# Optimization experiments

Hardware: AMD Instinct MI355X
Metric: run time of the kernel (lower is better)

## Reference

```python
import jax, jax.numpy as jnp
import numpy as np


def _maxpool2(t):
    # 2x2 max pool, stride 2. t: [B, C, H, W]
    B, C, H, W = t.shape
    return t.reshape(B, C, H // 2, 2, W // 2, 2).max(axis=(3, 5))


def setup_inputs() -> dict:
    key = jax.random.key(0)
    ks = jax.random.split(key, 5)
    B, C, H, W = 4, 64, 128, 128
    x = jax.random.normal(ks[0], (B, C, H, W), dtype=jnp.float32)
    w_theta = jax.random.normal(ks[1], (C // 8, C), dtype=jnp.float32) * (1.0 / np.sqrt(C))
    w_phi = jax.random.normal(ks[2], (C // 8, C), dtype=jnp.float32) * (1.0 / np.sqrt(C))
    w_g = jax.random.normal(ks[3], (C // 2, C), dtype=jnp.float32) * (1.0 / np.sqrt(C))
    w_o = jax.random.normal(ks[4], (C, C // 2), dtype=jnp.float32) * (1.0 / np.sqrt(C // 2))
    gamma = jnp.ones((1,), dtype=jnp.float32)
    return {"x": x, "w_theta": w_theta, "w_phi": w_phi, "w_g": w_g, "w_o": w_o, "gamma": gamma}


def reference(x, w_theta, w_phi, w_g, w_o, gamma):
    B, C, H, W = x.shape
    N = H * W
    # 1x1 convs (bias-free) are channel matmuls
    theta = jnp.einsum('oc,bchw->bohw', w_theta, x)            # [B, C/8, H, W]
    phi = _maxpool2(jnp.einsum('oc,bchw->bohw', w_phi, x))     # [B, C/8, H/2, W/2]
    g = _maxpool2(jnp.einsum('oc,bchw->bohw', w_g, x))         # [B, C/2, H/2, W/2]
    theta = theta.reshape(B, C // 8, N)                        # [B, C/8, N]
    phi = phi.reshape(B, C // 8, N // 4)                       # [B, C/8, N/4]
    g = g.reshape(B, C // 2, N // 4)                           # [B, C/2, N/4]
    # attention: no 1/sqrt(d) scaling in SAGAN
    scores = jnp.einsum('bcn,bcm->bnm', theta, phi)            # [B, N, N/4]
    beta = jax.nn.softmax(scores, axis=-1)
    attn = jnp.einsum('bcm,bnm->bcn', g, beta)                 # [B, C/2, N]
    o = jnp.einsum('oc,bcn->bon', w_o, attn).reshape(B, C, H, W)
    return gamma[0] * o + x
```

## Files before the change

kernel.cpp:

```cpp
#include <hip/hip_runtime.h>
#include <hip/hip_bf16.h>


typedef __attribute__((ext_vector_type(4))) float f32x4;
typedef __attribute__((ext_vector_type(8))) short s16x8;
typedef __attribute__((ext_vector_type(4))) short s16x4;

__device__ __forceinline__ unsigned short f32_bf16(float f) {
    unsigned int u = __float_as_uint(f);
    return (unsigned short)((u + 0x7fffu + ((u >> 16) & 1u)) >> 16);
}
__device__ __forceinline__ unsigned int pk_bf16(float a, float b) {
    return (unsigned int)f32_bf16(a) | ((unsigned int)f32_bf16(b) << 16);
}
__device__ __forceinline__ unsigned int pk_rh(float a, float b) {
    unsigned int au = __float_as_uint(a) + 0x8000u;
    unsigned int bu = __float_as_uint(b) + 0x8000u;
    return __builtin_amdgcn_perm(bu, au, 0x07060302u);
}
__device__ __forceinline__ unsigned int pk_tr(float a, float b) {
    return __builtin_amdgcn_perm(__float_as_uint(b), __float_as_uint(a), 0x07060302u);
}
__device__ __forceinline__ void async16(const void* g, void* l) {
    __builtin_amdgcn_global_load_lds(
        (const __attribute__((address_space(1))) unsigned int*)g,
        (__attribute__((address_space(3))) unsigned int*)l, 16, 0, 0);
}

__global__ __launch_bounds__(256) void proj_kernel(
    const float* __restrict__ x,
    const float* __restrict__ w_theta, const float* __restrict__ w_phi,
    const float* __restrict__ w_g,
    __hip_bfloat16* __restrict__ thG,
    __hip_bfloat16* __restrict__ phG,
    __hip_bfloat16* __restrict__ gG)
{
    __shared__ __align__(16) unsigned short x_s[128 * 72];
    int tid = threadIdx.x;
    int bx = blockIdx.x;
    int b = bx >> 7, mh = (bx >> 1) & 63, ph = bx & 1;

    {
        int cp = tid >> 3, s = tid & 7;
        const float* xb = x + ((size_t)b << 20) + (size_t)(2 * mh) * 128 + 64 * ph;
        const float* p0r = xb + ((size_t)(2 * cp) << 14);
        const float* p1r = p0r + (1 << 14);
#pragma unroll
        for (int py = 0; py < 2; py++)
#pragma unroll
            for (int t = 0; t < 2; t++) {
                int pxl = 4 * s + 32 * t;
                float4 a = *(const float4*)(p0r + py * 128 + pxl);
                float4 c = *(const float4*)(p1r + py * 128 + pxl);
                int pix = py * 64 + pxl;
                *(unsigned int*)&x_s[(pix + 0) * 72 + 2 * cp] = pk_rh(a.x, c.x);
                *(unsigned int*)&x_s[(pix + 1) * 72 + 2 * cp] = pk_rh(a.y, c.y);
                *(unsigned int*)&x_s[(pix + 2) * 72 + 2 * cp] = pk_rh(a.z, c.z);
                *(unsigned int*)&x_s[(pix + 3) * 72 + 2 * cp] = pk_rh(a.w, c.w);
            }
    }

    int lane = tid & 63, w = tid >> 6;
    int q = lane >> 4, nl = lane & 15;

    s16x8 A[3][2];
#pragma unroll
    for (int CT = 0; CT < 3; CT++) {
        const float* wsrc;
        float scale = 1.0f;
        if (CT == 0) {
            if (nl < 8) { wsrc = w_theta + nl * 64; scale = 1.44269504f; }
            else        { wsrc = w_phi + (nl - 8) * 64; }
        } else if (CT == 1) wsrc = w_g + nl * 64;
        else                wsrc = w_g + (16 + nl) * 64;
#pragma unroll
        for (int ks = 0; ks < 2; ks++) {
            const float4* p4 = (const float4*)(wsrc + 32 * ks + 8 * q);
            float4 a0 = p4[0], a1 = p4[1];
            s16x8 f;
            f[0] = (short)f32_bf16(a0.x * scale); f[1] = (short)f32_bf16(a0.y * scale);
            f[2] = (short)f32_bf16(a0.z * scale); f[3] = (short)f32_bf16(a0.w * scale);
            f[4] = (short)f32_bf16(a1.x * scale); f[5] = (short)f32_bf16(a1.y * scale);
            f[6] = (short)f32_bf16(a1.z * scale); f[7] = (short)f32_bf16(a1.w * scale);
            A[CT][ks] = f;
        }
    }
    __syncthreads();

    f32x4 acc[3][2];
#pragma unroll
    for (int ti = 0; ti < 2; ti++) {
        int tile = w + 4 * ti;
        const unsigned short* rb = x_s + (16 * tile + nl) * 72;
        s16x8 B0 = *(const s16x8*)(rb + 8 * q);
        s16x8 B1 = *(const s16x8*)(rb + 32 + 8 * q);
#pragma unroll
        for (int CT = 0; CT < 3; CT++) {
            f32x4 d = (f32x4){0.f, 0.f, 0.f, 0.f};
            d = __builtin_amdgcn_mfma_f32_16x16x32_bf16(A[CT][0], B0, d, 0, 0, 0);
            d = __builtin_amdgcn_mfma_f32_16x16x32_bf16(A[CT][1], B1, d, 0, 0, 0);
            acc[CT][ti] = d;
        }
    }

    if (q < 2) {
        unsigned short* thb = (unsigned short*)thG + ((size_t)b << 14) * 8;
#pragma unroll
        for (int ti = 0; ti < 2; ti++) {
            int n = (2 * mh + ti) * 128 + 64 * ph + 16 * w + nl;
            uint2 tv;
            tv.x = pk_bf16(acc[0][ti][0], acc[0][ti][1]);
            tv.y = pk_bf16(acc[0][ti][2], acc[0][ti][3]);
            *(uint2*)(thb + (size_t)n * 8 + 4 * q) = tv;
        }
    }

    float pool[3][4];
#pragma unroll
    for (int CT = 0; CT < 3; CT++)
#pragma unroll
        for (int r = 0; r < 4; r++) {
            float a = fmaxf(acc[CT][0][r], acc[CT][1][r]);
            pool[CT][r] = fmaxf(a, __shfl_xor(a, 1));
        }

    int mm = 8 * w + (nl >> 1);
    int mbase = mh * 64 + ph * 32;
    if ((nl & 1) == 0) {
        if (q >= 2) {
            uint2 pv;
            pv.x = pk_bf16(pool[0][0], pool[0][1]);
            pv.y = pk_bf16(pool[0][2], pool[0][3]);
            *(uint2*)((unsigned short*)phG + ((size_t)(b * 4096 + mbase + mm)) * 8 + (q - 2) * 4) = pv;
        }
        int p = 8 * ((mm >> 2) & 3) + 4 * ((mm >> 4) & 1) + (mm & 3);
        int mstore = mbase + p;
#pragma unroll
        for (int CT = 1; CT < 3; CT++)
#pragma unroll
            for (int r = 0; r < 4; r++) {
                int cg = 16 * (CT - 1) + 4 * q + r;
                ((unsigned short*)gG)[((size_t)(b * 32 + cg) << 12) + mstore] =
                    f32_bf16(pool[CT][r]);
            }
    }
}

__global__ __launch_bounds__(256) void attn_kernel(
    const __hip_bfloat16* __restrict__ thG, const __hip_bfloat16* __restrict__ phG,
    const __hip_bfloat16* __restrict__ gG,
    const float* __restrict__ w_o, const float* __restrict__ gamma,
    const float* __restrict__ x, float* __restrict__ out)
{
    __shared__ __align__(16) unsigned char smem[2 * 16384 + 2 * 4096];
    unsigned char* O_s = smem;

    int tid = threadIdx.x, lane = tid & 63, w = tid >> 6;
    int q = lane >> 4, nl = lane & 15;
    int bx = blockIdx.x;
    int b  = bx >> 7;
    int n0 = (bx & 127) << 7;
    int nw = n0 + w * 32;

    const unsigned short* thb = (const unsigned short*)thG + ((size_t)b << 14) * 8;
    const unsigned short* phb = (const unsigned short*)phG + ((size_t)b << 12) * 8;
    const unsigned short* ggb = (const unsigned short*)gG + ((size_t)b << 17);

    s16x8 BT0 = (s16x8){0, 0, 0, 0, 0, 0, 0, 0};
    s16x8 BT1 = (s16x8){0, 0, 0, 0, 0, 0, 0, 0};
    if (q == 0) {
        BT0 = *(const s16x8*)(thb + (size_t)(nw + nl) * 8);
        BT1 = *(const s16x8*)(thb + (size_t)(nw + 16 + nl) * 8);
    } else if (q == 1) {
        BT0[0] = (short)0xC167;
        BT1[0] = (short)0xC167;
    }
    s16x8 Fc = (s16x8){0, 0, 0, 0, 0, 0, 0, 0};
    if (q == 1) Fc[0] = (short)0x3F80;
    const s16x4 ONE4 = (s16x4){(short)0x3F80, (short)0x3F80, (short)0x3F80, (short)0x3F80};

    f32x4 acc00 = (f32x4){0.f, 0.f, 0.f, 0.f};
    f32x4 acc10 = (f32x4){0.f, 0.f, 0.f, 0.f};
    f32x4 acc01 = (f32x4){0.f, 0.f, 0.f, 0.f};
    f32x4 acc11 = (f32x4){0.f, 0.f, 0.f, 0.f};
    f32x4 accL0 = (f32x4){0.f, 0.f, 0.f, 0.f};
    f32x4 accL1 = (f32x4){0.f, 0.f, 0.f, 0.f};

    int r0 = 8 * w + (lane >> 5);
    const unsigned short* gsrc0 = ggb + ((size_t)(r0 + 0) << 12) + 8 * ((lane & 31) ^ (r0 + 0));
    const unsigned short* gsrc1 = ggb + ((size_t)(r0 + 2) << 12) + 8 * ((lane & 31) ^ (r0 + 2));
    const unsigned short* gsrc2 = ggb + ((size_t)(r0 + 4) << 12) + 8 * ((lane & 31) ^ (r0 + 4));
    const unsigned short* gsrc3 = ggb + ((size_t)(r0 + 6) << 12) + 8 * ((lane & 31) ^ (r0 + 6));
    const unsigned short* psrc  = phb + (size_t)(w * 64 + lane) * 8;
    unsigned char* ldsg0 = smem + w * 4096;
    unsigned char* ldsg1 = ldsg0 + 1024;
    unsigned char* ldsg2 = ldsg0 + 2048;
    unsigned char* ldsg3 = ldsg0 + 3072;
    unsigned char* ldsp  = smem + 32768 + w * 1024;

    async16(gsrc0, ldsg0);
    async16(gsrc1, ldsg1);
    async16(gsrc2, ldsg2);
    async16(gsrc3, ldsg3);
    async16(psrc, ldsp);
    __syncthreads();

    for (int st = 0; st < 16; st++) {
        const unsigned char* gcur = smem + (st & 1) * 16384;
        const unsigned char* pcur = smem + 32768 + (st & 1) * 4096;
        if (st < 15) {
            int mo = (st + 1) << 8;
            int nb = (st + 1) & 1;
            async16(gsrc0 + mo, ldsg0 + nb * 16384);
            async16(gsrc1 + mo, ldsg1 + nb * 16384);
            async16(gsrc2 + mo, ldsg2 + nb * 16384);
            async16(gsrc3 + mo, ldsg3 + nb * 16384);
            async16(psrc + (size_t)mo * 8, ldsp + nb * 4096);
        }
#pragma unroll
        for (int cc = 0; cc < 8; cc++) {
            int mloc = cc << 5;
            s16x8 F0 = Fc, F1 = Fc;
            if (q == 0) {
                F0 = *(const s16x8*)(pcur + (mloc + nl) * 16);
                F1 = *(const s16x8*)(pcur + (mloc + 16 + nl) * 16);
            }
            int t = (cc << 2) + q;
            s16x8 G0 = *(const s16x8*)(gcur + nl * 512 + ((t ^ nl) << 4));
            s16x8 G1 = *(const s16x8*)(gcur + (nl + 16) * 512 + ((t ^ (nl + 16)) << 4));

            f32x4 z = (f32x4){0.f, 0.f, 0.f, 0.f};
            f32x4 s00 = __builtin_amdgcn_mfma_f32_16x16x32_bf16(F0, BT0, z, 0, 0, 0);
            f32x4 s01 = __builtin_amdgcn_mfma_f32_16x16x32_bf16(F1, BT0, z, 0, 0, 0);
            f32x4 s10 = __builtin_amdgcn_mfma_f32_16x16x32_bf16(F0, BT1, z, 0, 0, 0);
            f32x4 s11 = __builtin_amdgcn_mfma_f32_16x16x32_bf16(F1, BT1, z, 0, 0, 0);

            float a0 = __builtin_amdgcn_exp2f(s00[0]);
            float a1 = __builtin_amdgcn_exp2f(s00[1]);
            float a2 = __builtin_amdgcn_exp2f(s00[2]);
            float a3 = __builtin_amdgcn_exp2f(s00[3]);
            float b0 = __builtin_amdgcn_exp2f(s01[0]);
            float b1 = __builtin_amdgcn_exp2f(s01[1]);
            float b2 = __builtin_amdgcn_exp2f(s01[2]);
            float b3 = __builtin_amdgcn_exp2f(s01[3]);
            float c0 = __builtin_amdgcn_exp2f(s10[0]);
            float c1 = __builtin_amdgcn_exp2f(s10[1]);
            float c2 = __builtin_amdgcn_exp2f(s10[2]);
            float c3 = __builtin_amdgcn_exp2f(s10[3]);
            float d0 = __builtin_amdgcn_exp2f(s11[0]);
            float d1 = __builtin_amdgcn_exp2f(s11[1]);
            float d2 = __builtin_amdgcn_exp2f(s11[2]);
            float d3 = __builtin_amdgcn_exp2f(s11[3]);

            uint2 u00 = make_uint2(pk_tr(a0, a1), pk_tr(a2, a3));
            uint2 u01 = make_uint2(pk_tr(b0, b1), pk_tr(b2, b3));
            uint2 u10 = make_uint2(pk_tr(c0, c1), pk_tr(c2, c3));
            uint2 u11 = make_uint2(pk_tr(d0, d1), pk_tr(d2, d3));
            s16x4 P00 = *(s16x4*)&u00;
            s16x4 P01 = *(s16x4*)&u01;
            s16x4 P10 = *(s16x4*)&u10;
            s16x4 P11 = *(s16x4*)&u11;

            accL0 = __builtin_amdgcn_mfma_f32_16x16x16bf16_1k(ONE4, P00, accL0, 0, 0, 0);
            accL0 = __builtin_amdgcn_mfma_f32_16x16x16bf16_1k(ONE4, P01, accL0, 0, 0, 0);
            accL1 = __builtin_amdgcn_mfma_f32_16x16x16bf16_1k(ONE4, P10, accL1, 0, 0, 0);
            accL1 = __builtin_amdgcn_mfma_f32_16x16x16bf16_1k(ONE4, P11, accL1, 0, 0, 0);

            s16x4 G0a = __builtin_shufflevector(G0, G0, 0, 1, 2, 3);
            s16x4 G0b = __builtin_shufflevector(G0, G0, 4, 5, 6, 7);
            s16x4 G1a = __builtin_shufflevector(G1, G1, 0, 1, 2, 3);
            s16x4 G1b = __builtin_shufflevector(G1, G1, 4, 5, 6, 7);
            acc00 = __builtin_amdgcn_mfma_f32_16x16x16bf16_1k(G0a, P00, acc00, 0, 0, 0);
            acc00 = __builtin_amdgcn_mfma_f32_16x16x16bf16_1k(G0b, P01, acc00, 0, 0, 0);
            acc10 = __builtin_amdgcn_mfma_f32_16x16x16bf16_1k(G1a, P00, acc10, 0, 0, 0);
            acc10 = __builtin_amdgcn_mfma_f32_16x16x16bf16_1k(G1b, P01, acc10, 0, 0, 0);
            acc01 = __builtin_amdgcn_mfma_f32_16x16x16bf16_1k(G0a, P10, acc01, 0, 0, 0);
            acc01 = __builtin_amdgcn_mfma_f32_16x16x16bf16_1k(G0b, P11, acc01, 0, 0, 0);
            acc11 = __builtin_amdgcn_mfma_f32_16x16x16bf16_1k(G1a, P10, acc11, 0, 0, 0);
            acc11 = __builtin_amdgcn_mfma_f32_16x16x16bf16_1k(G1b, P11, acc11, 0, 0, 0);
        }
        __syncthreads();
    }

    float li0 = 1.0f / accL0[0];
    float li1 = 1.0f / accL1[0];
    acc00 *= li0; acc10 *= li0;
    acc01 *= li1; acc11 *= li1;

    s16x8 WO[4];
#pragma unroll
    for (int g4 = 0; g4 < 4; g4++) {
        const float4* wr = (const float4*)(w_o + (size_t)(g4 * 16 + nl) * 32 + q * 8);
        float4 a0 = wr[0], a1 = wr[1];
        WO[g4][0] = (short)f32_bf16(a0.x); WO[g4][1] = (short)f32_bf16(a0.y);
        WO[g4][2] = (short)f32_bf16(a0.z); WO[g4][3] = (short)f32_bf16(a0.w);
        WO[g4][4] = (short)f32_bf16(a1.x); WO[g4][5] = (short)f32_bf16(a1.y);
        WO[g4][6] = (short)f32_bf16(a1.z); WO[g4][7] = (short)f32_bf16(a1.w);
    }
    float gam = gamma[0];

    int nloc0 = w * 32 + nl;
    int nloc1 = nloc0 + 16;
    {
        uint2 ov;
        ov.x = pk_bf16(acc00[0], acc00[1]); ov.y = pk_bf16(acc00[2], acc00[3]);
        *(uint2*)(O_s + nloc0 * 80 + q * 8) = ov;
        ov.x = pk_bf16(acc10[0], acc10[1]); ov.y = pk_bf16(acc10[2], acc10[3]);
        *(uint2*)(O_s + nloc0 * 80 + 32 + q * 8) = ov;
        ov.x = pk_bf16(acc01[0], acc01[1]); ov.y = pk_bf16(acc01[2], acc01[3]);
        *(uint2*)(O_s + nloc1 * 80 + q * 8) = ov;
        ov.x = pk_bf16(acc11[0], acc11[1]); ov.y = pk_bf16(acc11[2], acc11[3]);
        *(uint2*)(O_s + nloc1 * 80 + 32 + q * 8) = ov;
    }
    s16x8 OB0 = *(const s16x8*)(O_s + nloc0 * 80 + q * 16);
    s16x8 OB1 = *(const s16x8*)(O_s + nloc1 * 80 + q * 16);
#pragma unroll
    for (int g4 = 0; g4 < 4; g4++) {
        f32x4 e0 = (f32x4){0.f, 0.f, 0.f, 0.f};
        f32x4 e1 = (f32x4){0.f, 0.f, 0.f, 0.f};
        e0 = __builtin_amdgcn_mfma_f32_16x16x32_bf16(WO[g4], OB0, e0, 0, 0, 0);
        e1 = __builtin_amdgcn_mfma_f32_16x16x32_bf16(WO[g4], OB1, e1, 0, 0, 0);
#pragma unroll
        for (int r = 0; r < 4; r++) {
            int cc = g4 * 16 + q * 4 + r;
            size_t gi0 = (((size_t)(b * 64 + cc)) << 14) + nw + nl;
            out[gi0] = gam * e0[r] + x[gi0];
            size_t gi1 = gi0 + 16;
            out[gi1] = gam * e1[r] + x[gi1];
        }
    }
}

extern "C" void kernel_launch(void* const* d_in, const int* in_sizes, int n_in,
                              void* d_out, int out_size, void* d_ws, size_t ws_size,
                              hipStream_t stream) {
    const float* x       = (const float*)d_in[0];
    const float* w_theta = (const float*)d_in[1];
    const float* w_phi   = (const float*)d_in[2];
    const float* w_g     = (const float*)d_in[3];
    const float* w_o     = (const float*)d_in[4];
    const float* gamma   = (const float*)d_in[5];
    float* out = (float*)d_out;

    __hip_bfloat16* thG = (__hip_bfloat16*)d_ws;
    __hip_bfloat16* phG = thG + 524288;
    __hip_bfloat16* gG  = phG + 131072;

    proj_kernel<<<512, 256, 0, stream>>>(x, w_theta, w_phi, w_g, thG, phG, gG);
    attn_kernel<<<512, 256, 0, stream>>>(thG, phG, gG, w_o, gamma, x, out);
}
```

Measured before the change: 137.1 us.

## Switch attention inner loop to 32x32x16 MFMA and sum softmax denominator on VALU

Replaces the four 16x16x32 score MFMAs and eight 16x16x16 PV MFMAs per step with one 32x32x16 score MFMA and two 32x32x16 PV MFMAs over a single 16-register accumulator. The g pooling store permutation is changed to match the new operand layout. The row-sum of exp values now uses packed VALU adds plus a cross-half shuffle instead of extra MFMAs against a ones vector. The aim is fewer MFMA issues and less denominator overhead, at the cost of higher accumulator register pressure and a dependency on the new g layout being consistent.

```diff
diff --git a/kernel.cpp b/kernel.cpp
--- a/kernel.cpp
+++ b/kernel.cpp
@@ -2,9 +2,10 @@
 #include <hip/hip_bf16.h>
 
 
+typedef __attribute__((ext_vector_type(16))) float f32x16;
 typedef __attribute__((ext_vector_type(4))) float f32x4;
+typedef __attribute__((ext_vector_type(2))) float f32x2;
 typedef __attribute__((ext_vector_type(8))) short s16x8;
-typedef __attribute__((ext_vector_type(4))) short s16x4;
 
 __device__ __forceinline__ unsigned short f32_bf16(float f) {
     unsigned int u = __float_as_uint(f);
@@ -133,7 +134,7 @@
             pv.y = pk_bf16(pool[0][2], pool[0][3]);
             *(uint2*)((unsigned short*)phG + ((size_t)(b * 4096 + mbase + mm)) * 8 + (q - 2) * 4) = pv;
         }
-        int p = 8 * ((mm >> 2) & 3) + 4 * ((mm >> 4) & 1) + (mm & 3);
+        int p = 16 * ((mm >> 4) & 1) + 8 * ((mm >> 2) & 1) + 4 * ((mm >> 3) & 1) + (mm & 3);
         int mstore = mbase + p;
 #pragma unroll
         for (int CT = 1; CT < 3; CT++)
@@ -157,6 +158,7 @@
 
     int tid = threadIdx.x, lane = tid & 63, w = tid >> 6;
     int q = lane >> 4, nl = lane & 15;
+    int c31 = lane & 31, h = lane >> 5;
     int bx = blockIdx.x;
     int b  = bx >> 7;
     int n0 = (bx & 127) << 7;
@@ -166,25 +168,14 @@
     const unsigned short* phb = (const unsigned short*)phG + ((size_t)b << 12) * 8;
     const unsigned short* ggb = (const unsigned short*)gG + ((size_t)b << 17);
 
-    s16x8 BT0 = (s16x8){0, 0, 0, 0, 0, 0, 0, 0};
-    s16x8 BT1 = (s16x8){0, 0, 0, 0, 0, 0, 0, 0};
-    if (q == 0) {
-        BT0 = *(const s16x8*)(thb + (size_t)(nw + nl) * 8);
-        BT1 = *(const s16x8*)(thb + (size_t)(nw + 16 + nl) * 8);
-    } else if (q == 1) {
-        BT0[0] = (short)0xC167;
-        BT1[0] = (short)0xC167;
-    }
+    s16x8 BT = (s16x8){0, 0, 0, 0, 0, 0, 0, 0};
+    if (h == 0) BT = *(const s16x8*)(thb + (size_t)(nw + c31) * 8);
+    else        BT[0] = (short)0xC167;
     s16x8 Fc = (s16x8){0, 0, 0, 0, 0, 0, 0, 0};
-    if (q == 1) Fc[0] = (short)0x3F80;
-    const s16x4 ONE4 = (s16x4){(short)0x3F80, (short)0x3F80, (short)0x3F80, (short)0x3F80};
-
-    f32x4 acc00 = (f32x4){0.f, 0.f, 0.f, 0.f};
-    f32x4 acc10 = (f32x4){0.f, 0.f, 0.f, 0.f};
-    f32x4 acc01 = (f32x4){0.f, 0.f, 0.f, 0.f};
-    f32x4 acc11 = (f32x4){0.f, 0.f, 0.f, 0.f};
-    f32x4 accL0 = (f32x4){0.f, 0.f, 0.f, 0.f};
-    f32x4 accL1 = (f32x4){0.f, 0.f, 0.f, 0.f};
+    if (h == 1) Fc[0] = (short)0x3F80;
+
+    f32x16 acc = {};
+    f32x2  l2 = (f32x2){0.f, 0.f};
 
     int r0 = 8 * w + (lane >> 5);
     const unsigned short* gsrc0 = ggb + ((size_t)(r0 + 0) << 12) + 8 * ((lane & 31) ^ (r0 + 0));
@@ -218,74 +209,57 @@
             async16(psrc + (size_t)mo * 8, ldsp + nb * 4096);
         }
 #pragma unroll
-        for (int cc = 0; cc < 8; cc++) {
-            int mloc = cc << 5;
-            s16x8 F0 = Fc, F1 = Fc;
-            if (q == 0) {
-                F0 = *(const s16x8*)(pcur + (mloc + nl) * 16);
-                F1 = *(const s16x8*)(pcur + (mloc + 16 + nl) * 16);
-            }
-            int t = (cc << 2) + q;
-            s16x8 G0 = *(const s16x8*)(gcur + nl * 512 + ((t ^ nl) << 4));
-            s16x8 G1 = *(const s16x8*)(gcur + (nl + 16) * 512 + ((t ^ (nl + 16)) << 4));
-
-            f32x4 z = (f32x4){0.f, 0.f, 0.f, 0.f};
-            f32x4 s00 = __builtin_amdgcn_mfma_f32_16x16x32_bf16(F0, BT0, z, 0, 0, 0);
-            f32x4 s01 = __builtin_amdgcn_mfma_f32_16x16x32_bf16(F1, BT0, z, 0, 0, 0);
-            f32x4 s10 = __builtin_amdgcn_mfma_f32_16x16x32_bf16(F0, BT1, z, 0, 0, 0);
-            f32x4 s11 = __builtin_amdgcn_mfma_f32_16x16x32_bf16(F1, BT1, z, 0, 0, 0);
-
-            float a0 = __builtin_amdgcn_exp2f(s00[0]);
-            float a1 = __builtin_amdgcn_exp2f(s00[1]);
-            float a2 = __builtin_amdgcn_exp2f(s00[2]);
-            float a3 = __builtin_amdgcn_exp2f(s00[3]);
-            float b0 = __builtin_amdgcn_exp2f(s01[0]);
-            float b1 = __builtin_amdgcn_exp2f(s01[1]);
-            float b2 = __builtin_amdgcn_exp2f(s01[2]);
-            float b3 = __builtin_amdgcn_exp2f(s01[3]);
-            float c0 = __builtin_amdgcn_exp2f(s10[0]);
-            float c1 = __builtin_amdgcn_exp2f(s10[1]);
-            float c2 = __builtin_amdgcn_exp2f(s10[2]);
-            float c3 = __builtin_amdgcn_exp2f(s10[3]);
-            float d0 = __builtin_amdgcn_exp2f(s11[0]);
-            float d1 = __builtin_amdgcn_exp2f(s11[1]);
-            float d2 = __builtin_amdgcn_exp2f(s11[2]);
-            float d3 = __builtin_amdgcn_exp2f(s11[3]);
-
-            uint2 u00 = make_uint2(pk_tr(a0, a1), pk_tr(a2, a3));
-            uint2 u01 = make_uint2(pk_tr(b0, b1), pk_tr(b2, b3));
-            uint2 u10 = make_uint2(pk_tr(c0, c1), pk_tr(c2, c3));
-            uint2 u11 = make_uint2(pk_tr(d0, d1), pk_tr(d2, d3));
-            s16x4 P00 = *(s16x4*)&u00;
-            s16x4 P01 = *(s16x4*)&u01;
-            s16x4 P10 = *(s16x4*)&u10;
-            s16x4 P11 = *(s16x4*)&u11;
-
-            accL0 = __builtin_amdgcn_mfma_f32_16x16x16bf16_1k(ONE4, P00, accL0, 0, 0, 0);
-            accL0 = __builtin_amdgcn_mfma_f32_16x16x16bf16_1k(ONE4, P01, accL0, 0, 0, 0);
-            accL1 = __builtin_amdgcn_mfma_f32_16x16x16bf16_1k(ONE4, P10, accL1, 0, 0, 0);
-            accL1 = __builtin_amdgcn_mfma_f32_16x16x16bf16_1k(ONE4, P11, accL1, 0, 0, 0);
-
-            s16x4 G0a = __builtin_shufflevector(G0, G0, 0, 1, 2, 3);
-            s16x4 G0b = __builtin_shufflevector(G0, G0, 4, 5, 6, 7);
-            s16x4 G1a = __builtin_shufflevector(G1, G1, 0, 1, 2, 3);
-            s16x4 G1b = __builtin_shufflevector(G1, G1, 4, 5, 6, 7);
-            acc00 = __builtin_amdgcn_mfma_f32_16x16x16bf16_1k(G0a, P00, acc00, 0, 0, 0);
-            acc00 = __builtin_amdgcn_mfma_f32_16x16x16bf16_1k(G0b, P01, acc00, 0, 0, 0);
-            acc10 = __builtin_amdgcn_mfma_f32_16x16x16bf16_1k(G1a, P00, acc10, 0, 0, 0);
-            acc10 = __builtin_amdgcn_mfma_f32_16x16x16bf16_1k(G1b, P01, acc10, 0, 0, 0);
-            acc01 = __builtin_amdgcn_mfma_f32_16x16x16bf16_1k(G0a, P10, acc01, 0, 0, 0);
-            acc01 = __builtin_amdgcn_mfma_f32_16x16x16bf16_1k(G0b, P11, acc01, 0, 0, 0);
-            acc11 = __builtin_amdgcn_mfma_f32_16x16x16bf16_1k(G1a, P10, acc11, 0, 0, 0);
-            acc11 = __builtin_amdgcn_mfma_f32_16x16x16bf16_1k(G1b, P11, acc11, 0, 0, 0);
+        for (int t8 = 0; t8 < 8; t8++) {
+            int mloc = t8 << 5;
+            s16x8 F = Fc;
+            if (h == 0) F = *(const s16x8*)(pcur + (mloc + c31) * 16);
+            int s0 = (t8 << 2) + h;
+            s16x8 G1 = *(const s16x8*)(gcur + c31 * 512 + (((s0 + 0) ^ c31) << 4));
+            s16x8 G2 = *(const s16x8*)(gcur + c31 * 512 + (((s0 + 2) ^ c31) << 4));
+
+            f32x16 z = {};
+            f32x16 S = __builtin_amdgcn_mfma_f32_32x32x16_bf16(F, BT, z, 0, 0, 0);
+
+            float p0  = __builtin_amdgcn_exp2f(S[0]);
+            float p1  = __builtin_amdgcn_exp2f(S[1]);
+            float p2  = __builtin_amdgcn_exp2f(S[2]);
+            float p3  = __builtin_amdgcn_exp2f(S[3]);
+            float p4  = __builtin_amdgcn_exp2f(S[4]);
+            float p5  = __builtin_amdgcn_exp2f(S[5]);
+            float p6  = __builtin_amdgcn_exp2f(S[6]);
+            float p7  = __builtin_amdgcn_exp2f(S[7]);
+            float p8  = __builtin_amdgcn_exp2f(S[8]);
+            float p9  = __builtin_amdgcn_exp2f(S[9]);
+            float p10 = __builtin_amdgcn_exp2f(S[10]);
+            float p11 = __builtin_amdgcn_exp2f(S[11]);
+            float p12 = __builtin_amdgcn_exp2f(S[12]);
+            float p13 = __builtin_amdgcn_exp2f(S[13]);
+            float p14 = __builtin_amdgcn_exp2f(S[14]);
+            float p15 = __builtin_amdgcn_exp2f(S[15]);
+
+            f32x2 u0 = (f32x2){p0, p1} + (f32x2){p2, p3};
+            f32x2 u1 = (f32x2){p4, p5} + (f32x2){p6, p7};
+            f32x2 u2 = (f32x2){p8, p9} + (f32x2){p10, p11};
+            f32x2 u3 = (f32x2){p12, p13} + (f32x2){p14, p15};
+            l2 += (u0 + u1) + (u2 + u3);
+
+            uint4 ub1 = make_uint4(pk_tr(p0, p1), pk_tr(p2, p3),
+                                   pk_tr(p4, p5), pk_tr(p6, p7));
+            uint4 ub2 = make_uint4(pk_tr(p8, p9), pk_tr(p10, p11),
+                                   pk_tr(p12, p13), pk_tr(p14, p15));
+            s16x8 B1 = *(s16x8*)&ub1;
+            s16x8 B2 = *(s16x8*)&ub2;
+
+            acc = __builtin_amdgcn_mfma_f32_32x32x16_bf16(G1, B1, acc, 0, 0, 0);
+            acc = __builtin_amdgcn_mfma_f32_32x32x16_bf16(G2, B2, acc, 0, 0, 0);
         }
         __syncthreads();
     }
 
-    float li0 = 1.0f / accL0[0];
-    float li1 = 1.0f / accL1[0];
-    acc00 *= li0; acc10 *= li0;
-    acc01 *= li1; acc11 *= li1;
+    float l = l2[0] + l2[1];
+    l += __shfl_xor(l, 32);
+    float linv = 1.0f / l;
+    acc *= linv;
 
     s16x8 WO[4];
 #pragma unroll
@@ -299,19 +273,18 @@
     }
     float gam = gamma[0];
 
+    int nloc = w * 32 + c31;
+    {
+#pragma unroll
+        for (int g2 = 0; g2 < 4; g2++) {
+            uint2 ov;
+            ov.x = pk_bf16(acc[4 * g2 + 0], acc[4 * g2 + 1]);
+            ov.y = pk_bf16(acc[4 * g2 + 2], acc[4 * g2 + 3]);
+            *(uint2*)(O_s + nloc * 80 + 16 * g2 + 8 * h) = ov;
+        }
+    }
     int nloc0 = w * 32 + nl;
     int nloc1 = nloc0 + 16;
-    {
-        uint2 ov;
-        ov.x = pk_bf16(acc00[0], acc00[1]); ov.y = pk_bf16(acc00[2], acc00[3]);
-        *(uint2*)(O_s + nloc0 * 80 + q * 8) = ov;
-        ov.x = pk_bf16(acc10[0], acc10[1]); ov.y = pk_bf16(acc10[2], acc10[3]);
-        *(uint2*)(O_s + nloc0 * 80 + 32 + q * 8) = ov;
-        ov.x = pk_bf16(acc01[0], acc01[1]); ov.y = pk_bf16(acc01[2], acc01[3]);
-        *(uint2*)(O_s + nloc1 * 80 + q * 8) = ov;
-        ov.x = pk_bf16(acc11[0], acc11[1]); ov.y = pk_bf16(acc11[2], acc11[3]);
-        *(uint2*)(O_s + nloc1 * 80 + 32 + q * 8) = ov;
-    }
     s16x8 OB0 = *(const s16x8*)(O_s + nloc0 * 80 + q * 16);
     s16x8 OB1 = *(const s16x8*)(O_s + nloc1 * 80 + q * 16);
 #pragma unroll
```

Result: faster. 127.5 us (-7.0%).
